# Kernel tuning notes

Hardware: AMD Instinct MI355X
Metric: run time of the kernel (lower is better)

## Reference

```python
import jax, jax.numpy as jnp
import numpy as np
from jax import lax
from jax.scipy.special import logsumexp

NEG = -1e9  # finite stand-in for -inf masking (grad-safe)
TEMP = 0.1
GAMMA = 2.0
EPS_DICE = 1e-6
EPS_GRAD = 1e-6
TINY_THRESH = 2048
FG_IDX = 1
MAX_TINY = 1024
MAX_OTHER = 4096
MIN_TINY = 16


def setup_inputs() -> dict:
    key = jax.random.key(0)
    k1, k2, k3, k4, k5 = jax.random.split(key, 5)
    B, C, H, W = 8, 5, 512, 512
    Cf, D = 32, 256
    logits = jax.random.normal(k1, (B, C, H, W), dtype=jnp.float32)
    # targets: no random class-1 pixels; plant a 32x32 (=1024 px <= 2048) fg patch per image
    t = jax.random.randint(k2, (B, H, W), 0, C)
    t = jnp.where(t == FG_IDX, 0, t)
    t = t.at[:, 100:132, 100:132].set(FG_IDX)
    targets = t.astype(jnp.int32)
    projected_features = jax.random.normal(k3, (B, Cf, H, W), dtype=jnp.float32)
    embeddings = jax.random.normal(k4, (B, D), dtype=jnp.float32)
    cls_targets = jax.random.randint(k5, (B,), 0, 3).astype(jnp.int32)
    return {"logits": logits, "targets": targets,
            "projected_features": projected_features,
            "embeddings": embeddings, "cls_targets": cls_targets}


def _l2norm(x, axis=-1):
    return x / jnp.maximum(jnp.linalg.norm(x, axis=axis, keepdims=True), 1e-12)


def _sobel(x):
    # x: [B,1,H,W] -> (|grad|) using 3x3 sobel kernels, padding 1
    kx = jnp.array([[-1., 0., 1.], [-2., 0., 2.], [-1., 0., 1.]], x.dtype).reshape(1, 1, 3, 3)
    ky = jnp.array([[-1., -2., -1.], [0., 0., 0.], [1., 2., 1.]], x.dtype).reshape(1, 1, 3, 3)
    dn = ('NCHW', 'OIHW', 'NCHW')
    gx = lax.conv_general_dilated(x, kx, (1, 1), [(1, 1), (1, 1)], dimension_numbers=dn)
    gy = lax.conv_general_dilated(x, ky, (1, 1), [(1, 1), (1, 1)], dimension_numbers=dn)
    return jnp.sqrt(gx * gx + gy * gy + EPS_GRAD)


def _first_n_indices(mask_flat, n):
    # deterministic replacement for randperm sampling: pick first n True indices
    N = mask_flat.shape[0]
    keys = jnp.where(mask_flat, -jnp.arange(N, dtype=jnp.float32), -jnp.inf)
    _, idx = lax.top_k(keys, n)
    count = jnp.sum(mask_flat)
    valid = jnp.arange(n) < jnp.minimum(count, n)
    return idx, valid


def reference(logits, targets, projected_features, embeddings, cls_targets):
    B, C, H, W = logits.shape
    tgt = targets.astype(jnp.int32)

    # --- cross entropy (per-pixel) ---
    logp = jax.nn.log_softmax(logits, axis=1)                      # [B,C,H,W]
    ce = -jnp.take_along_axis(logp, tgt[:, None], axis=1)[:, 0]    # [B,H,W]
    ce_loss = ce.mean()

    # --- focal (alpha=None) ---
    pt = jnp.exp(-ce)
    focal = (jnp.clip(1.0 - pt, 0.0, 1.0) ** GAMMA) * ce
    focal_loss_v = focal.mean()

    # --- soft dice ---
    probs = jnp.exp(logp)                                          # softmax
    one_hot = jax.nn.one_hot(tgt, C, dtype=probs.dtype, axis=1)    # [B,C,H,W]
    inter = jnp.sum(probs * one_hot, axis=(0, 2, 3))
    denom = jnp.sum(probs + one_hot, axis=(0, 2, 3))
    dice = (2.0 * inter + EPS_DICE) / (denom + EPS_DICE)
    dice_loss = 1.0 - dice.mean()

    # --- sobel gradient boundary (C>2 -> target_fg = targets>0) ---
    pred_fg = probs[:, FG_IDX:FG_IDX + 1]                          # [B,1,H,W]
    target_fg = (tgt > 0).astype(logits.dtype)[:, None]
    grad_loss = jnp.abs(_sobel(pred_fg) - _sobel(target_fg)).mean()

    # --- tiny-object pixel contrastive ---
    fg_mask = (tgt == FG_IDX)
    fg_per_img = fg_mask.reshape(B, -1).sum(axis=1)
    tiny_img = (fg_per_img > 0) & (fg_per_img <= TINY_THRESH)
    tiny_fg = fg_mask & tiny_img[:, None, None]                    # [B,H,W]
    flat_tiny = tiny_fg.reshape(-1)
    tiny_idx, tiny_valid = _first_n_indices(flat_tiny, MAX_TINY)
    other_idx, other_valid = _first_n_indices(~flat_tiny, MAX_OTHER)
    Cf = projected_features.shape[1]
    feats = projected_features.transpose(0, 2, 3, 1).reshape(-1, Cf)
    t_emb = _l2norm(feats[tiny_idx])                               # [MAX_TINY,Cf]
    o_emb = _l2norm(feats[other_idx])                              # [MAX_OTHER,Cf]
    sim_t = t_emb @ t_emb.T / TEMP
    eye = jnp.eye(MAX_TINY, dtype=bool)
    sim_t = jnp.where(eye | ~tiny_valid[None, :], NEG, sim_t)
    sim_o = jnp.where(~other_valid[None, :], NEG, t_emb @ o_emb.T / TEMP)
    log_num = logsumexp(sim_t, axis=1)
    log_den = logsumexp(jnp.concatenate([sim_t, sim_o], axis=1), axis=1)
    per = -(log_num - log_den)
    n_t = jnp.maximum(jnp.sum(tiny_valid), 1)
    tiny_loss = jnp.sum(jnp.where(tiny_valid, per, 0.0)) / n_t
    enabled = tiny_img.any() & (jnp.sum(tiny_fg) >= MIN_TINY)
    tiny_loss = jnp.where(enabled, tiny_loss, 0.0)

    # --- class-aware embedding contrastive (single-label path) ---
    emb = _l2norm(embeddings)                                      # [B,D]
    labels = cls_targets.reshape(-1)
    sim = emb @ emb.T / max(TEMP, 1e-6)
    eyeB = jnp.eye(B, dtype=bool)
    pos = (labels[:, None] == labels[None, :]) & ~eyeB
    valid = pos.any(axis=1)
    lse_pos = logsumexp(jnp.where(pos, sim, NEG), axis=1)
    lse_all = logsumexp(jnp.where(~eyeB, sim, NEG), axis=1)
    per_a = -(lse_pos - lse_all)
    n_v = jnp.maximum(jnp.sum(valid), 1)
    contrastive_main = jnp.sum(jnp.where(valid, per_a, 0.0)) / n_v
    # pairwise BCE fallback (used only if no valid anchors)
    cos = jnp.clip(emb @ emb.T, -1.0, 1.0)
    p01 = (cos + 1.0) * 0.5
    tsim = (labels[:, None] == labels[None, :]).astype(jnp.float32)
    bce = -(tsim * jnp.clip(jnp.log(p01), -100.0, None)
            + (1.0 - tsim) * jnp.clip(jnp.log(1.0 - p01), -100.0, None))
    off = ~eyeB
    bce_fb = jnp.sum(jnp.where(off, bce, 0.0)) / jnp.sum(off)
    cls_contrastive = jnp.where(valid.any(), contrastive_main, bce_fb)

    total = ce_loss + dice_loss + focal_loss_v + grad_loss + tiny_loss + cls_contrastive
    return total
```

## Files before the change

kernel.cpp:

```cpp
#include <hip/hip_runtime.h>
#include <hip/hip_bf16.h>
#include <math.h>

#define Bq   8
#define Cc   5
#define Hh   512
#define Ww   512
#define HW   262144
#define NPIX 2097152
#define CF   32
#define NROWS 4096
#define MAXT 1024
#define MAXO 4096
#define NBLK 1024
#define GSTRIDE 262144
#define GITER 8

#define FO_ACC    0
#define IO_ROWCNT 32
#define FO_ST     4128
#define FO_SO     5152
#define Z_ELEMS   6176
#define IO_PREFIX 6176
#define IO_SCAL   10272
#define IO_TIDX   10288
#define IO_OIDX   11312
#define FO_TEMB   15408
#define FO_OEMB   48176
#define FO_PART   179248
#define FO_GPART  197680
#define FO_PRED   198704
#define WS_ELEMS  2295856

__device__ __forceinline__ float wave_sum(float v) {
  #pragma unroll
  for (int off = 32; off > 0; off >>= 1) v += __shfl_xor(v, off);
  return v;
}

__global__ __launch_bounds__(256) void k_main(const float* __restrict__ logits,
                                              const int* __restrict__ targets,
                                              float* __restrict__ wsf,
                                              int* __restrict__ wsi) {
  int tid = threadIdx.x;
  float acc[18];
  #pragma unroll
  for (int k = 0; k < 18; k++) acc[k] = 0.0f;
  int base = blockIdx.x * 256 + tid;
  for (int it = 0; it < GITER; it++) {
    int idx = base + it * GSTRIDE;
    int b = idx >> 18;
    int rem = idx & (HW - 1);
    const float* lp = logits + (size_t)b * (Cc * HW) + rem;
    float l0 = lp[0], l1 = lp[HW], l2 = lp[2 * HW], l3 = lp[3 * HW], l4 = lp[4 * HW];
    float m = fmaxf(fmaxf(fmaxf(l0, l1), fmaxf(l2, l3)), l4);
    float e0 = __expf(l0 - m), e1 = __expf(l1 - m), e2 = __expf(l2 - m),
          e3 = __expf(l3 - m), e4 = __expf(l4 - m);
    float se = e0 + e1 + e2 + e3 + e4;
    float inv = 1.0f / se;
    float p0 = e0 * inv, p1 = e1 * inv, p2 = e2 * inv, p3 = e3 * inv, p4 = e4 * inv;
    int t = targets[idx];
    float lt = t == 0 ? l0 : t == 1 ? l1 : t == 2 ? l2 : t == 3 ? l3 : l4;
    float pt = t == 0 ? p0 : t == 1 ? p1 : t == 2 ? p2 : t == 3 ? p3 : p4;
    float ce = __logf(se) + m - lt;
    float om = fminf(fmaxf(1.0f - pt, 0.0f), 1.0f);
    float focal = om * om * ce;
    wsf[FO_PRED + idx] = p1;
    unsigned long long mask = __ballot(t == 1);
    if (((tid & 63) == 0) && mask)
      atomicAdd(&wsi[IO_ROWCNT + (idx >> 9)], __popcll(mask));
    acc[0] += ce; acc[1] += focal;
    acc[3] += (t == 0) ? pt : 0.0f;
    acc[4] += (t == 1) ? pt : 0.0f;
    acc[5] += (t == 2) ? pt : 0.0f;
    acc[6] += (t == 3) ? pt : 0.0f;
    acc[7] += (t == 4) ? pt : 0.0f;
    acc[8] += p0; acc[9] += p1; acc[10] += p2; acc[11] += p3; acc[12] += p4;
    acc[13] += (t == 0) ? 1.0f : 0.0f;
    acc[14] += (t == 1) ? 1.0f : 0.0f;
    acc[15] += (t == 2) ? 1.0f : 0.0f;
    acc[16] += (t == 3) ? 1.0f : 0.0f;
    acc[17] += (t == 4) ? 1.0f : 0.0f;
  }
  __shared__ float red[4][18];
  #pragma unroll
  for (int k = 0; k < 18; k++) acc[k] = wave_sum(acc[k]);
  int lane = tid & 63, wv = tid >> 6;
  if (lane == 0) {
    #pragma unroll
    for (int k = 0; k < 18; k++) red[wv][k] = acc[k];
  }
  __syncthreads();
  if (tid < 18) {
    float s = red[0][tid] + red[1][tid] + red[2][tid] + red[3][tid];
    wsf[FO_PART + tid * NBLK + blockIdx.x] = s;
  }
}

__global__ __launch_bounds__(256) void k_sobel(const int* __restrict__ targets,
                                               const float* __restrict__ pred,
                                               float* __restrict__ wsf) {
  int tid = threadIdx.x;
  float vsum = 0.0f;
  int base = blockIdx.x * 256 + tid;
  for (int it = 0; it < GITER; it++) {
    int idx = base + it * GSTRIDE;
    int b = idx >> 18;
    int hw = idx & (HW - 1);
    int h = hw >> 9, w = hw & (Ww - 1);
    const float* pb = pred + (size_t)b * HW;
    const int* tb = targets + (size_t)b * HW;
    float pp[9], tf[9];
    #pragma unroll
    for (int dh = 0; dh < 3; dh++) {
      int hh = h + dh - 1;
      bool hin = (hh >= 0) & (hh < Hh);
      #pragma unroll
      for (int dw = 0; dw < 3; dw++) {
        int wc = w + dw - 1;
        bool in = hin & (wc >= 0) & (wc < Ww);
        float pv = 0.0f, tv = 0.0f;
        if (in) {
          int o = hh * Ww + wc;
          pv = pb[o];
          tv = (tb[o] > 0) ? 1.0f : 0.0f;
        }
        pp[dh * 3 + dw] = pv;
        tf[dh * 3 + dw] = tv;
      }
    }
    float gxp = (pp[2] + 2.0f * pp[5] + pp[8]) - (pp[0] + 2.0f * pp[3] + pp[6]);
    float gyp = (pp[6] + 2.0f * pp[7] + pp[8]) - (pp[0] + 2.0f * pp[1] + pp[2]);
    float gp = sqrtf(gxp * gxp + gyp * gyp + 1e-6f);
    float gxt = (tf[2] + 2.0f * tf[5] + tf[8]) - (tf[0] + 2.0f * tf[3] + tf[6]);
    float gyt = (tf[6] + 2.0f * tf[7] + tf[8]) - (tf[0] + 2.0f * tf[1] + tf[2]);
    float gt = sqrtf(gxt * gxt + gyt * gyt + 1e-6f);
    vsum += fabsf(gp - gt);
  }
  vsum = wave_sum(vsum);
  __shared__ float red[4];
  int lane = tid & 63, wv = tid >> 6;
  if (lane == 0) red[wv] = vsum;
  __syncthreads();
  if (tid == 0) wsf[FO_GPART + blockIdx.x] = red[0] + red[1] + red[2] + red[3];
}

__global__ __launch_bounds__(256) void k_scan(int* __restrict__ wsi,
                                              float* __restrict__ wsf) {
  __shared__ int ssum[256];
  __shared__ int stimg[8];
  __shared__ int sc[256];
  __shared__ float fred[4][18];
  __shared__ float gred[4];
  int tid = threadIdx.x;
  int lane = tid & 63, wv = tid >> 6;

  float ls[18];
  #pragma unroll
  for (int k = 0; k < 18; k++) {
    const float* p = wsf + FO_PART + k * NBLK + tid;
    ls[k] = p[0] + p[256] + p[512] + p[768];
  }
  #pragma unroll
  for (int k = 0; k < 18; k++) ls[k] = wave_sum(ls[k]);
  if (lane == 0) {
    #pragma unroll
    for (int k = 0; k < 18; k++) fred[wv][k] = ls[k];
  }
  {
    const float* p = wsf + FO_GPART + tid;
    float g = p[0] + p[256] + p[512] + p[768];
    g = wave_sum(g);
    if (lane == 0) gred[wv] = g;
  }
  __syncthreads();
  if (tid < 18) {
    float s = fred[0][tid] + fred[1][tid] + fred[2][tid] + fred[3][tid];
    if (tid == 2) s = gred[0] + gred[1] + gred[2] + gred[3];
    wsf[FO_ACC + tid] = s;
  }

  int base = tid * 16;
  int loc[16];
  int s = 0;
  #pragma unroll
  for (int k = 0; k < 16; k++) { loc[k] = wsi[IO_ROWCNT + base + k]; s += loc[k]; }
  ssum[tid] = s;
  __syncthreads();
  if (tid < 8) {
    int tot = 0;
    for (int u = 0; u < 32; u++) tot += ssum[tid * 32 + u];
    stimg[tid] = (tot > 0 && tot <= 2048) ? 1 : 0;
  }
  __syncthreads();
  int timg = stimg[tid >> 5];
  int ms = timg ? s : 0;
  sc[tid] = ms;
  __syncthreads();
  for (int off = 1; off < 256; off <<= 1) {
    int add = (tid >= off) ? sc[tid - off] : 0;
    __syncthreads();
    sc[tid] += add;
    __syncthreads();
  }
  int run = sc[tid] - ms;
  #pragma unroll
  for (int k = 0; k < 16; k++) {
    wsi[IO_PREFIX + base + k] = run;
    run += timg ? loc[k] : 0;
  }
  if (tid == 255) wsi[IO_SCAL + 0] = sc[255];
  if (tid < 8) wsi[IO_SCAL + 2 + tid] = stimg[tid];
  if (tid == 0) {
    int anyf = 0;
    for (int u = 0; u < 8; u++) anyf |= stimg[u];
    wsi[IO_SCAL + 1] = anyf;
  }
}

__global__ __launch_bounds__(512) void k_widx(const int* __restrict__ targets,
                                              int* __restrict__ wsi) {
  int r = blockIdx.x;
  int tid = threadIdx.x;
  int b = r >> 9;
  int timg = wsi[IO_SCAL + 2 + b];
  int trc = timg ? wsi[IO_ROWCNT + r] : 0;
  int p = wsi[IO_PREFIX + r];
  int q = (r << 9) - p;
  bool need_t = (trc > 0) && (p < MAXT);
  bool need_o = (q < MAXO) && (trc < 512);
  if (!need_t && !need_o) return;
  int i = (r << 9) + tid;
  int t = targets[i];
  bool f = (timg != 0) && (t == 1);
  unsigned long long mask = __ballot(f ? 1 : 0);
  int lane = tid & 63, wv = tid >> 6;
  int lpfx = __popcll(mask & ((1ull << lane) - 1ull));
  __shared__ int wt[8];
  if (lane == 0) wt[wv] = __popcll(mask);
  __syncthreads();
  int woff = 0;
  for (int u = 0; u < wv; u++) woff += wt[u];
  int local = woff + lpfx;
  if (f) {
    int pos = p + local;
    if (pos < MAXT) wsi[IO_TIDX + pos] = i;
  } else {
    int fpos = q + (tid - local);
    if (fpos < MAXO) wsi[IO_OIDX + fpos] = i;
  }
}

__global__ __launch_bounds__(256) void k_gather(const float* __restrict__ pf,
                                                const int* __restrict__ wsi,
                                                float* __restrict__ wsf) {
  int tid = threadIdx.x;
  int g = blockIdx.x * 8 + (tid >> 5);
  int lane = tid & 31;
  int cnt = wsi[IO_SCAL + 0];
  int cnt_t = cnt < MAXT ? cnt : MAXT;
  long cfal = (long)NPIX - (long)cnt;
  int cnt_o = cfal > MAXO ? MAXO : (int)cfal;
  int idx;
  float* dst;
  if (g < MAXT) {
    dst = wsf + FO_TEMB + (size_t)g * 32;
    idx = (g < cnt_t) ? wsi[IO_TIDX + g] : -1;
  } else {
    int go = g - MAXT;
    dst = wsf + FO_OEMB + (size_t)go * 32;
    idx = (go < cnt_o) ? wsi[IO_OIDX + go] : -1;
  }
  float v = 0.0f;
  if (idx >= 0) {
    int b = idx >> 18;
    int rem = idx & (HW - 1);
    v = pf[((size_t)b * CF + lane) * HW + rem];
  }
  float ss = v * v;
  #pragma unroll
  for (int off = 16; off > 0; off >>= 1) ss += __shfl_xor(ss, off, 32);
  float nrm = fmaxf(sqrtf(ss), 1e-12f);
  dst[lane] = v / nrm;
}

__global__ __launch_bounds__(256) void k_sim(float* __restrict__ wsf,
                                             const int* __restrict__ wsi) {
  int tid = threadIdx.x;
  int rb = blockIdx.x / 80;
  int cc = blockIdx.x % 80;
  int j = rb * 256 + tid;
  const float* temb = wsf + FO_TEMB;
  const float* oemb = wsf + FO_OEMB;
  float rv[32];
  const float4* r4 = (const float4*)(temb + (size_t)j * 32);
  #pragma unroll
  for (int k = 0; k < 8; k++) {
    float4 x = r4[k];
    rv[4 * k + 0] = x.x; rv[4 * k + 1] = x.y; rv[4 * k + 2] = x.z; rv[4 * k + 3] = x.w;
  }
  int cnt = wsi[IO_SCAL + 0];
  int cnt_t = cnt < MAXT ? cnt : MAXT;
  long cfal = (long)NPIX - (long)cnt;
  int cnt_o = cfal > MAXO ? MAXO : (int)cfal;
  int c0 = cc * 64;
  bool is_t = (c0 < MAXT);
  const float* cbase = is_t ? (temb + (size_t)c0 * 32) : (oemb + (size_t)(c0 - MAXT) * 32);
  int climit = is_t ? (cnt_t - c0) : (cnt_o - (c0 - MAXT));
  float s = 0.0f;
  for (int c = 0; c < 64; c += 4) {
    const float* cv0 = cbase + (c + 0) * 32;
    const float* cv1 = cbase + (c + 1) * 32;
    const float* cv2 = cbase + (c + 2) * 32;
    const float* cv3 = cbase + (c + 3) * 32;
    float d0 = 0.0f, d1 = 0.0f, d2 = 0.0f, d3 = 0.0f;
    #pragma unroll
    for (int k = 0; k < 32; k++) {
      float r = rv[k];
      d0 = fmaf(r, cv0[k], d0);
      d1 = fmaf(r, cv1[k], d1);
      d2 = fmaf(r, cv2[k], d2);
      d3 = fmaf(r, cv3[k], d3);
    }
    bool m0 = ((c + 0) >= climit) || (is_t && ((c0 + c + 0) == j));
    bool m1 = ((c + 1) >= climit) || (is_t && ((c0 + c + 1) == j));
    bool m2 = ((c + 2) >= climit) || (is_t && ((c0 + c + 2) == j));
    bool m3 = ((c + 3) >= climit) || (is_t && ((c0 + c + 3) == j));
    s += m0 ? 0.0f : __expf(d0 * 10.0f);
    s += m1 ? 0.0f : __expf(d1 * 10.0f);
    s += m2 ? 0.0f : __expf(d2 * 10.0f);
    s += m3 ? 0.0f : __expf(d3 * 10.0f);
  }
  atomicAdd(&wsf[(is_t ? FO_ST : FO_SO) + j], s);
}

__global__ __launch_bounds__(256) void k_final(const float* __restrict__ emb,
                                               const int* __restrict__ clst,
                                               const float* __restrict__ wsf,
                                               const int* __restrict__ wsi,
                                               float* __restrict__ out) {
  __shared__ float e[8 * 256];
  __shared__ float sdot[64];
  __shared__ float sred[4];
  __shared__ float s_pera[8];
  __shared__ int s_val[8];
  __shared__ float s_bce[8];
  int tid = threadIdx.x;

  int cnt = wsi[IO_SCAL + 0];
  int vt = cnt < MAXT ? cnt : MAXT;
  float ts = 0.0f;
  for (int jj = tid; jj < vt; jj += 256) {
    float a = wsf[FO_ST + jj];
    float c2 = wsf[FO_SO + jj];
    ts += __logf(a + c2) - __logf(a);
  }
  ts = wave_sum(ts);
  if ((tid & 63) == 0) sred[tid >> 6] = ts;
  __syncthreads();

  for (int k = tid; k < 2048; k += 256) e[k] = emb[k];
  __syncthreads();
  int row = tid >> 5, lane = tid & 31;
  float ss = 0.0f;
  for (int k = lane; k < 256; k += 32) { float v = e[row * 256 + k]; ss += v * v; }
  #pragma unroll
  for (int off = 16; off > 0; off >>= 1) ss += __shfl_xor(ss, off, 32);
  float invn = 1.0f / fmaxf(sqrtf(ss), 1e-12f);
  for (int k = lane; k < 256; k += 32) e[row * 256 + k] *= invn;
  __syncthreads();
  if (tid < 64) {
    int i = tid >> 3, jc = tid & 7;
    float d = 0.0f;
    for (int k = 0; k < 256; k++) d = fmaf(e[i * 256 + k], e[jc * 256 + k], d);
    sdot[tid] = d;
  }
  __syncthreads();
  if (tid < 8) {
    int li = clst[tid];
    float spos = 0.0f, sall = 0.0f, bce = 0.0f;
    int haspos = 0;
    for (int jc = 0; jc < 8; jc++) {
      if (jc == tid) continue;
      float d = sdot[tid * 8 + jc];
      float ex = __expf(d * 10.0f);
      sall += ex;
      int same = (clst[jc] == li) ? 1 : 0;
      if (same) { spos += ex; haspos = 1; }
      float cosv = fminf(fmaxf(d, -1.0f), 1.0f);
      float p01 = (cosv + 1.0f) * 0.5f;
      float lpv = fmaxf(__logf(p01), -100.0f);
      float lnv = fmaxf(__logf(1.0f - p01), -100.0f);
      bce += -(same ? lpv : lnv);
    }
    s_pera[tid] = __logf(sall) - __logf(spos);
    s_val[tid] = haspos;
    s_bce[tid] = bce;
  }
  __syncthreads();
  if (tid == 0) {
    int nv = 0;
    float sm = 0.0f, sb = 0.0f;
    for (int i = 0; i < 8; i++) {
      if (s_val[i]) { nv++; sm += s_pera[i]; }
      sb += s_bce[i];
    }
    float cls = (nv > 0) ? (sm / (float)nv) : (sb / 56.0f);
    float invN = 1.0f / (float)NPIX;
    float ce_l = wsf[0] * invN;
    float focal_l = wsf[1] * invN;
    float grad_l = wsf[2] * invN;
    float dsum = 0.0f;
    for (int c = 0; c < 5; c++)
      dsum += (2.0f * wsf[3 + c] + 1e-6f) / (wsf[8 + c] + wsf[13 + c] + 1e-6f);
    float dice_l = 1.0f - dsum * 0.2f;
    int anyt = wsi[IO_SCAL + 1];
    bool enabled = (anyt != 0) && (cnt >= 16);
    float tiny_total = sred[0] + sred[1] + sred[2] + sred[3];
    int n_t = vt > 1 ? vt : 1;
    float tiny_l = enabled ? (tiny_total / (float)n_t) : 0.0f;
    out[0] = ce_l + dice_l + focal_l + grad_l + tiny_l + cls;
  }
}

extern "C" void kernel_launch(void* const* d_in, const int* in_sizes, int n_in,
                              void* d_out, int out_size, void* d_ws, size_t ws_size,
                              hipStream_t stream) {
  (void)in_sizes; (void)n_in; (void)out_size; (void)ws_size;
  const float* logits = (const float*)d_in[0];
  const int* targets = (const int*)d_in[1];
  const float* pf = (const float*)d_in[2];
  const float* emb = (const float*)d_in[3];
  const int* clst = (const int*)d_in[4];
  float* out = (float*)d_out;
  float* wsf = (float*)d_ws;
  int* wsi = (int*)d_ws;

  hipMemsetAsync(d_ws, 0, Z_ELEMS * 4, stream);
  hipLaunchKernelGGL(k_main, dim3(NBLK), dim3(256), 0, stream, logits, targets, wsf, wsi);
  hipLaunchKernelGGL(k_sobel, dim3(NBLK), dim3(256), 0, stream, targets, wsf + FO_PRED, wsf);
  hipLaunchKernelGGL(k_scan, dim3(1), dim3(256), 0, stream, wsi, wsf);
  hipLaunchKernelGGL(k_widx, dim3(NROWS), dim3(512), 0, stream, targets, wsi);
  hipLaunchKernelGGL(k_gather, dim3(5120 / 8), dim3(256), 0, stream, pf, wsi, wsf);
  hipLaunchKernelGGL(k_sim, dim3(320), dim3(256), 0, stream, wsf, wsi);
  hipLaunchKernelGGL(k_final, dim3(1), dim3(256), 0, stream, emb, clst, wsf, wsi, out);
}
```

Baseline: 392.5 us.

## Vectorize main loss pass and tile Sobel pass by rows with float4 loads

The main per-pixel kernel now handles 4 contiguous pixels per thread with float4/int4 loads, doubling the block count and summing foreground counts per wave before one atomic per wave. The Sobel kernel is restructured so each thread computes 8 adjacent pixels of one row from three loaded row segments, reusing neighbours in registers instead of doing 9 scalar loads per pixel. The scan kernel reduces over 2048 partials. This targets memory-bound load inefficiency and redundant stencil loads, at the cost of more registers per thread.

```diff
diff --git a/kernel.cpp b/kernel.cpp
--- a/kernel.cpp
+++ b/kernel.cpp
@@ -12,9 +12,8 @@
 #define NROWS 4096
 #define MAXT 1024
 #define MAXO 4096
-#define NBLK 1024
-#define GSTRIDE 262144
-#define GITER 8
+#define NBLKM 2048
+#define NBLKS 1024
 
 #define FO_ACC    0
 #define IO_ROWCNT 32
@@ -28,9 +27,9 @@
 #define FO_TEMB   15408
 #define FO_OEMB   48176
 #define FO_PART   179248
-#define FO_GPART  197680
-#define FO_PRED   198704
-#define WS_ELEMS  2295856
+#define FO_GPART  216112
+#define FO_PRED   217136
+#define WS_ELEMS  2314288
 
 __device__ __forceinline__ float wave_sum(float v) {
   #pragma unroll
@@ -43,33 +42,44 @@
                                               float* __restrict__ wsf,
                                               int* __restrict__ wsi) {
   int tid = threadIdx.x;
+  int idx = (blockIdx.x * 256 + tid) << 2;
+  int b = idx >> 18;
+  int rem = idx & (HW - 1);
+  const float* lp = logits + (size_t)b * (Cc * HW) + rem;
+  float4 c0 = *(const float4*)(lp);
+  float4 c1 = *(const float4*)(lp + HW);
+  float4 c2 = *(const float4*)(lp + 2 * HW);
+  float4 c3 = *(const float4*)(lp + 3 * HW);
+  float4 c4 = *(const float4*)(lp + 4 * HW);
+  int4 ti = *(const int4*)(targets + idx);
+  float l[5][4] = {{c0.x, c0.y, c0.z, c0.w},
+                   {c1.x, c1.y, c1.z, c1.w},
+                   {c2.x, c2.y, c2.z, c2.w},
+                   {c3.x, c3.y, c3.z, c3.w},
+                   {c4.x, c4.y, c4.z, c4.w}};
+  int ta[4] = {ti.x, ti.y, ti.z, ti.w};
   float acc[18];
   #pragma unroll
   for (int k = 0; k < 18; k++) acc[k] = 0.0f;
-  int base = blockIdx.x * 256 + tid;
-  for (int it = 0; it < GITER; it++) {
-    int idx = base + it * GSTRIDE;
-    int b = idx >> 18;
-    int rem = idx & (HW - 1);
-    const float* lp = logits + (size_t)b * (Cc * HW) + rem;
-    float l0 = lp[0], l1 = lp[HW], l2 = lp[2 * HW], l3 = lp[3 * HW], l4 = lp[4 * HW];
+  float pout[4];
+  int fgc = 0;
+  #pragma unroll
+  for (int px = 0; px < 4; px++) {
+    float l0 = l[0][px], l1 = l[1][px], l2 = l[2][px], l3 = l[3][px], l4 = l[4][px];
     float m = fmaxf(fmaxf(fmaxf(l0, l1), fmaxf(l2, l3)), l4);
     float e0 = __expf(l0 - m), e1 = __expf(l1 - m), e2 = __expf(l2 - m),
           e3 = __expf(l3 - m), e4 = __expf(l4 - m);
     float se = e0 + e1 + e2 + e3 + e4;
     float inv = 1.0f / se;
     float p0 = e0 * inv, p1 = e1 * inv, p2 = e2 * inv, p3 = e3 * inv, p4 = e4 * inv;
-    int t = targets[idx];
+    int t = ta[px];
     float lt = t == 0 ? l0 : t == 1 ? l1 : t == 2 ? l2 : t == 3 ? l3 : l4;
     float pt = t == 0 ? p0 : t == 1 ? p1 : t == 2 ? p2 : t == 3 ? p3 : p4;
     float ce = __logf(se) + m - lt;
     float om = fminf(fmaxf(1.0f - pt, 0.0f), 1.0f);
-    float focal = om * om * ce;
-    wsf[FO_PRED + idx] = p1;
-    unsigned long long mask = __ballot(t == 1);
-    if (((tid & 63) == 0) && mask)
-      atomicAdd(&wsi[IO_ROWCNT + (idx >> 9)], __popcll(mask));
-    acc[0] += ce; acc[1] += focal;
+    pout[px] = p1;
+    fgc += (t == 1) ? 1 : 0;
+    acc[0] += ce; acc[1] += om * om * ce;
     acc[3] += (t == 0) ? pt : 0.0f;
     acc[4] += (t == 1) ? pt : 0.0f;
     acc[5] += (t == 2) ? pt : 0.0f;
@@ -82,10 +92,16 @@
     acc[16] += (t == 3) ? 1.0f : 0.0f;
     acc[17] += (t == 4) ? 1.0f : 0.0f;
   }
+  float4 po = {pout[0], pout[1], pout[2], pout[3]};
+  *(float4*)(wsf + FO_PRED + idx) = po;
+  #pragma unroll
+  for (int off = 32; off > 0; off >>= 1) fgc += __shfl_xor(fgc, off);
+  int lane = tid & 63, wv = tid >> 6;
+  if (lane == 0 && fgc) atomicAdd(&wsi[IO_ROWCNT + (idx >> 9)], fgc);
+
   __shared__ float red[4][18];
   #pragma unroll
   for (int k = 0; k < 18; k++) acc[k] = wave_sum(acc[k]);
-  int lane = tid & 63, wv = tid >> 6;
   if (lane == 0) {
     #pragma unroll
     for (int k = 0; k < 18; k++) red[wv][k] = acc[k];
@@ -93,7 +109,7 @@
   __syncthreads();
   if (tid < 18) {
     float s = red[0][tid] + red[1][tid] + red[2][tid] + red[3][tid];
-    wsf[FO_PART + tid * NBLK + blockIdx.x] = s;
+    wsf[FO_PART + tid * NBLKM + blockIdx.x] = s;
   }
 }
 
@@ -101,46 +117,56 @@
                                                const float* __restrict__ pred,
                                                float* __restrict__ wsf) {
   int tid = threadIdx.x;
-  float vsum = 0.0f;
-  int base = blockIdx.x * 256 + tid;
-  for (int it = 0; it < GITER; it++) {
-    int idx = base + it * GSTRIDE;
-    int b = idx >> 18;
-    int hw = idx & (HW - 1);
-    int h = hw >> 9, w = hw & (Ww - 1);
-    const float* pb = pred + (size_t)b * HW;
-    const int* tb = targets + (size_t)b * HW;
-    float pp[9], tf[9];
-    #pragma unroll
-    for (int dh = 0; dh < 3; dh++) {
-      int hh = h + dh - 1;
-      bool hin = (hh >= 0) & (hh < Hh);
+  int h = blockIdx.x * 4 + (tid >> 6);
+  int w0 = (tid & 63) << 3;
+  int b = h >> 9, hl = h & 511;
+  const float* pb = pred + (size_t)b * HW;
+  const int* tb = targets + (size_t)b * HW;
+  float P[3][10], T[3][10];
+  #pragma unroll
+  for (int r = 0; r < 3; r++) {
+    int hr = hl + r - 1;
+    bool v = (hr >= 0) & (hr < Hh);
+    if (v) {
+      int base = (hr << 9) + w0;
+      float4 a = *(const float4*)(pb + base);
+      float4 bb = *(const float4*)(pb + base + 4);
+      P[r][1] = a.x;  P[r][2] = a.y;  P[r][3] = a.z;  P[r][4] = a.w;
+      P[r][5] = bb.x; P[r][6] = bb.y; P[r][7] = bb.z; P[r][8] = bb.w;
+      P[r][0] = (w0 > 0)   ? pb[base - 1] : 0.0f;
+      P[r][9] = (w0 < 504) ? pb[base + 8] : 0.0f;
+      int4 u = *(const int4*)(tb + base);
+      int4 w = *(const int4*)(tb + base + 4);
+      T[r][1] = (u.x > 0) ? 1.0f : 0.0f; T[r][2] = (u.y > 0) ? 1.0f : 0.0f;
+      T[r][3] = (u.z > 0) ? 1.0f : 0.0f; T[r][4] = (u.w > 0) ? 1.0f : 0.0f;
+      T[r][5] = (w.x > 0) ? 1.0f : 0.0f; T[r][6] = (w.y > 0) ? 1.0f : 0.0f;
+      T[r][7] = (w.z > 0) ? 1.0f : 0.0f; T[r][8] = (w.w > 0) ? 1.0f : 0.0f;
+      T[r][0] = (w0 > 0   && tb[base - 1] > 0) ? 1.0f : 0.0f;
+      T[r][9] = (w0 < 504 && tb[base + 8] > 0) ? 1.0f : 0.0f;
+    } else {
       #pragma unroll
-      for (int dw = 0; dw < 3; dw++) {
-        int wc = w + dw - 1;
-        bool in = hin & (wc >= 0) & (wc < Ww);
-        float pv = 0.0f, tv = 0.0f;
-        if (in) {
-          int o = hh * Ww + wc;
-          pv = pb[o];
-          tv = (tb[o] > 0) ? 1.0f : 0.0f;
-        }
-        pp[dh * 3 + dw] = pv;
-        tf[dh * 3 + dw] = tv;
-      }
+      for (int c = 0; c < 10; c++) { P[r][c] = 0.0f; T[r][c] = 0.0f; }
     }
-    float gxp = (pp[2] + 2.0f * pp[5] + pp[8]) - (pp[0] + 2.0f * pp[3] + pp[6]);
-    float gyp = (pp[6] + 2.0f * pp[7] + pp[8]) - (pp[0] + 2.0f * pp[1] + pp[2]);
+  }
+  float s = 0.0f;
+  #pragma unroll
+  for (int px = 0; px < 8; px++) {
+    float gxp = (P[0][px + 2] - P[0][px]) + 2.0f * (P[1][px + 2] - P[1][px]) +
+                (P[2][px + 2] - P[2][px]);
+    float gyp = (P[2][px] + 2.0f * P[2][px + 1] + P[2][px + 2]) -
+                (P[0][px] + 2.0f * P[0][px + 1] + P[0][px + 2]);
     float gp = sqrtf(gxp * gxp + gyp * gyp + 1e-6f);
-    float gxt = (tf[2] + 2.0f * tf[5] + tf[8]) - (tf[0] + 2.0f * tf[3] + tf[6]);
-    float gyt = (tf[6] + 2.0f * tf[7] + tf[8]) - (tf[0] + 2.0f * tf[1] + tf[2]);
+    float gxt = (T[0][px + 2] - T[0][px]) + 2.0f * (T[1][px + 2] - T[1][px]) +
+                (T[2][px + 2] - T[2][px]);
+    float gyt = (T[2][px] + 2.0f * T[2][px + 1] + T[2][px + 2]) -
+                (T[0][px] + 2.0f * T[0][px + 1] + T[0][px + 2]);
     float gt = sqrtf(gxt * gxt + gyt * gyt + 1e-6f);
-    vsum += fabsf(gp - gt);
-  }
-  vsum = wave_sum(vsum);
+    s += fabsf(gp - gt);
+  }
+  s = wave_sum(s);
   __shared__ float red[4];
   int lane = tid & 63, wv = tid >> 6;
-  if (lane == 0) red[wv] = vsum;
+  if (lane == 0) red[wv] = s;
   __syncthreads();
   if (tid == 0) wsf[FO_GPART + blockIdx.x] = red[0] + red[1] + red[2] + red[3];
 }
@@ -158,8 +184,11 @@
   float ls[18];
   #pragma unroll
   for (int k = 0; k < 18; k++) {
-    const float* p = wsf + FO_PART + k * NBLK + tid;
-    ls[k] = p[0] + p[256] + p[512] + p[768];
+    const float* p = wsf + FO_PART + k * NBLKM + tid;
+    float v = 0.0f;
+    #pragma unroll
+    for (int i = 0; i < 8; i++) v += p[i * 256];
+    ls[k] = v;
   }
   #pragma unroll
   for (int k = 0; k < 18; k++) ls[k] = wave_sum(ls[k]);
@@ -437,8 +466,8 @@
   int* wsi = (int*)d_ws;
 
   hipMemsetAsync(d_ws, 0, Z_ELEMS * 4, stream);
-  hipLaunchKernelGGL(k_main, dim3(NBLK), dim3(256), 0, stream, logits, targets, wsf, wsi);
-  hipLaunchKernelGGL(k_sobel, dim3(NBLK), dim3(256), 0, stream, targets, wsf + FO_PRED, wsf);
+  hipLaunchKernelGGL(k_main, dim3(NBLKM), dim3(256), 0, stream, logits, targets, wsf, wsi);
+  hipLaunchKernelGGL(k_sobel, dim3(NBLKS), dim3(256), 0, stream, targets, wsf + FO_PRED, wsf);
   hipLaunchKernelGGL(k_scan, dim3(1), dim3(256), 0, stream, wsi, wsf);
   hipLaunchKernelGGL(k_widx, dim3(NROWS), dim3(512), 0, stream, targets, wsi);
   hipLaunchKernelGGL(k_gather, dim3(5120 / 8), dim3(256), 0, stream, pf, wsi, wsf);
```

Result: faster. 381.7 us (-2.7%).
